# Kernel tuning notes

Hardware: AMD Instinct MI355X
Metric: run time of the kernel (lower is better)

## Reference

```python
import jax, jax.numpy as jnp
import numpy as np

N_NODES = 10000
N_EDGES = 640000
NODE_DIM = 128
EDGE_DIM = 32
OUT_DIM = 128


def setup_inputs() -> dict:
    key = jax.random.key(0)
    k_h, k_e, k_ef, k_w1, k_w2 = jax.random.split(key, 5)
    h = jax.random.normal(k_h, (N_NODES, NODE_DIM), dtype=jnp.float32)
    edge_index = jax.random.randint(k_e, (2, N_EDGES), 0, N_NODES, dtype=jnp.int64)
    edge_features = jax.random.normal(k_ef, (N_EDGES, EDGE_DIM), dtype=jnp.float32)
    in_dim = 2 * NODE_DIM + EDGE_DIM
    # Kaiming-ish init scale for realism
    W1 = jax.random.normal(k_w1, (in_dim, OUT_DIM), dtype=jnp.float32) / np.sqrt(in_dim)
    b1 = jnp.zeros((OUT_DIM,), dtype=jnp.float32)
    W2 = jax.random.normal(k_w2, (OUT_DIM, OUT_DIM), dtype=jnp.float32) / np.sqrt(OUT_DIM)
    b2 = jnp.zeros((OUT_DIM,), dtype=jnp.float32)
    return {"h": h, "edge_index": edge_index, "edge_features": edge_features,
            "n": N_NODES, "W1": W1, "b1": b1, "W2": W2, "b2": b2}


def reference(h, edge_index, edge_features, n, W1, b1, W2, b2):
    rows, cols = edge_index[0], edge_index[1]
    # gather source/target node features + edge features -> [E, 2*node_dim+edge_dim]
    msg_input = jnp.concatenate([h[rows], h[cols], edge_features], axis=-1)
    hidden = jax.nn.relu(msg_input @ W1 + b1)   # [E, out_dim]
    messages = hidden @ W2 + b2                 # [E, out_dim]
    # scatter-add messages onto destination rows -> [n, out_dim]
    out = jax.ops.segment_sum(messages, rows, num_segments=n)
    return out
```

## Files before the change

### kernel.cpp

```cpp
#include <hip/hip_runtime.h>
#include <hip/hip_bf16.h>


typedef __attribute__((ext_vector_type(8))) short bf16x8;
typedef __attribute__((ext_vector_type(4))) float f32x4;

#define ND 128
#define ED 32
#define CH 64

__device__ __forceinline__ short f2bf(float x) {
  unsigned int u = __float_as_uint(x);
  unsigned int r = (u + 0x7FFFu + ((u >> 16) & 1u)) >> 16;
  return (short)r;
}

__device__ __forceinline__ float bf2f(short s) {
  return __uint_as_float(((unsigned int)(unsigned short)s) << 16);
}

__device__ __forceinline__ f32x4 bf8lo(bf16x8 v) {
  f32x4 r;
  #pragma unroll
  for (int j = 0; j < 4; ++j) r[j] = bf2f(v[j]);
  return r;
}
__device__ __forceinline__ f32x4 bf8hi(bf16x8 v) {
  f32x4 r;
  #pragma unroll
  for (int j = 0; j < 4; ++j) r[j] = bf2f(v[4 + j]);
  return r;
}

__device__ __forceinline__ int load_idx(const void* ei, long long i, int is64) {
  return is64 ? (int)((const long long*)ei)[i] : ((const int*)ei)[i];
}

__device__ __forceinline__ int swz(int c) {
  int ct = c >> 4, cc = c & 15;
  return (ct >> 2) * 64 + (cc >> 2) * 16 + (ct & 3) * 4 + (cc & 3);
}

__global__ __launch_bounds__(256) void prep_kernel(
    const float* __restrict__ W1, const float* __restrict__ W2,
    const unsigned int* __restrict__ ei, short* __restrict__ w12t,
    short* __restrict__ w1eA, short* __restrict__ w2t, int* __restrict__ flag) {
  if (blockIdx.x == 0 && threadIdx.x == 0) {
    int is64 = 1;
    for (int i = 0; i < 16; ++i)
      if (ei[2 * i + 1] != 0u) is64 = 0;
    flag[0] = is64;
  }
  int t = blockIdx.x * blockDim.x + threadIdx.x;
  if (t < 256 * 128) {
    int np = t >> 7, k = t & 127;
    float v = (np < 128) ? W1[k * 128 + np] : W1[(128 + k) * 128 + (np - 128)];
    w12t[t] = f2bf(v);
  }
  if (t < 128 * 128) {
    int n = t >> 7, k = t & 127;
    w2t[t] = f2bf(W2[k * 128 + n]);
  }
  if (t < 8 * 64 * 8) {
    int ct = t >> 9, lane = (t >> 3) & 63, j = t & 7;
    int li = lane & 15, lg = lane >> 4;
    w1eA[t] = f2bf(W1[(256 + lg * 8 + j) * 128 + ct * 16 + li]);
  }
}

__global__ void hist_kernel(const void* __restrict__ ei, const int* __restrict__ flag,
                            int* __restrict__ counts, int* __restrict__ rank, int E) {
  int e = blockIdx.x * blockDim.x + threadIdx.x;
  if (e >= E) return;
  int r = load_idx(ei, e, flag[0]);
  rank[e] = atomicAdd(&counts[r], 1);
}

__global__ __launch_bounds__(1024) void scan_kernel(const int* __restrict__ counts,
                                                    int* __restrict__ row_ptr, int n) {
  __shared__ int wtot[16];
  int tid = threadIdx.x;
  int lane = tid & 63, w = tid >> 6;
  int base_i = tid * 16;
  int c[16];
  int tot = 0;
  #pragma unroll
  for (int j = 0; j < 16; ++j) {
    int i = base_i + j;
    c[j] = (i < n) ? counts[i] : 0;
    tot += c[j];
  }
  int x = tot;
  #pragma unroll
  for (int d = 1; d < 64; d <<= 1) {
    int t = __shfl_up(x, d);
    if (lane >= d) x += t;
  }
  if (lane == 63) wtot[w] = x;
  __syncthreads();
  if (w == 0) {
    int y = (lane < 16) ? wtot[lane] : 0;
    #pragma unroll
    for (int d = 1; d < 16; d <<= 1) {
      int t = __shfl_up(y, d);
      if (lane >= d) y += t;
    }
    if (lane < 16) wtot[lane] = y;
  }
  __syncthreads();
  int waveoff = (w == 0) ? 0 : wtot[w - 1];
  int run = waveoff + x - tot;
  if (tid == 0) row_ptr[0] = 0;
  #pragma unroll
  for (int j = 0; j < 16; ++j) {
    int i = base_i + j;
    if (i < n) {
      run += c[j];
      row_ptr[i + 1] = run;
    }
  }
}

__global__ __launch_bounds__(256, 4) void scatter_sg_kernel(
    const void* __restrict__ ei, const int* __restrict__ flag,
    const int* __restrict__ row_ptr, const int* __restrict__ rank,
    const float* __restrict__ h, const short* __restrict__ w12t,
    const float* __restrict__ b1, int2* __restrict__ ec, int2* __restrict__ cb,
    float* __restrict__ s2, short* __restrict__ g2, int N, int E, int nchunks) {
  int b = blockIdx.x;
  int SGB = (N + 63) >> 6;
  int SCB = (E + 255) >> 8;
  if (b < SGB) {
    int lane = threadIdx.x & 63, w = threadIdx.x >> 6;
    int li = lane & 15, lg = lane >> 4;
    int base = b * 64 + w * 16;
    int rowm = base + li;
    if (rowm >= N) rowm = N - 1;
    float breg[8];
    #pragma unroll
    for (int nt = 0; nt < 8; ++nt) breg[nt] = b1[nt * 16 + li];
    f32x4 acc[16];
    #pragma unroll
    for (int nt = 0; nt < 16; ++nt) acc[nt] = (f32x4){0.f, 0.f, 0.f, 0.f};
    #pragma unroll
    for (int kc = 0; kc < 4; ++kc) {
      f32x4 f0 = *(const f32x4*)(h + (size_t)rowm * ND + kc * 32 + lg * 8);
      f32x4 f1 = *(const f32x4*)(h + (size_t)rowm * ND + kc * 32 + lg * 8 + 4);
      bf16x8 a;
      #pragma unroll
      for (int j = 0; j < 4; ++j) { a[j] = f2bf(f0[j]); a[4 + j] = f2bf(f1[j]); }
      #pragma unroll
      for (int nt = 0; nt < 16; ++nt) {
        bf16x8 bb = *(const bf16x8*)(w12t + (nt * 16 + li) * 128 + kc * 32 + lg * 8);
        acc[nt] = __builtin_amdgcn_mfma_f32_16x16x32_bf16(a, bb, acc[nt], 0, 0, 0);
      }
    }
    #pragma unroll
    for (int nt = 0; nt < 16; ++nt)
      #pragma unroll
      for (int r = 0; r < 4; ++r) {
        int row = base + lg * 4 + r;
        if (row < N) {
          if (nt < 8) {
            s2[(size_t)row * 128 + swz(nt * 16 + li)] = acc[nt][r] + breg[nt];
          } else {
            g2[(size_t)row * 128 + swz((nt - 8) * 16 + li)] = f2bf(acc[nt][r]);
          }
        }
      }
  } else if (b < SGB + SCB) {
    int e = (b - SGB) * 256 + threadIdx.x;
    if (e < E) {
      int f = flag[0];
      int r = load_idx(ei, e, f);
      int c = load_idx(ei, (long long)E + e, f);
      ec[row_ptr[r] + rank[e]] = make_int2(e, c);
    }
  } else {
    int k = (b - SGB - SCB) * 256 + threadIdx.x;
    if (k < nchunks) {
      int t0 = k * CH, t1 = t0 + CH;
      int lo = 0, hi = N;
      while (lo < hi) { int mid = (lo + hi) >> 1; if (row_ptr[mid] < t0) lo = mid + 1; else hi = mid; }
      int na = lo;
      hi = N;
      while (lo < hi) { int mid = (lo + hi) >> 1; if (row_ptr[mid] < t1) lo = mid + 1; else hi = mid; }
      cb[k] = make_int2(na, lo);
    }
  }
}

__global__ __launch_bounds__(128) void layer1_kernel(
    const float* __restrict__ s2, const short* __restrict__ g2,
    const float* __restrict__ ef, const int2* __restrict__ ec,
    const short* __restrict__ w1eA, const int* __restrict__ row_ptr,
    const int2* __restrict__ cb, float* __restrict__ hsum) {
  int2 bounds = cb[blockIdx.x];
  int na = bounds.x, nb = bounds.y;
  if (na >= nb) return;
  int lane = threadIdx.x & 63;
  int w = threadIdx.x >> 6;
  int li = lane & 15, lg = lane >> 4;

  bf16x8 wa[4];
  #pragma unroll
  for (int nt = 0; nt < 4; ++nt)
    wa[nt] = *(const bf16x8*)(w1eA + ((w * 4 + nt) * 64 + lane) * 8);

  for (int n = na; n < nb; ++n) {
    int rp = row_ptr[n], rpe = row_ptr[n + 1];
    int deg = rpe - rp;
    f32x4 sreg[4];
    #pragma unroll
    for (int nt = 0; nt < 4; ++nt)
      sreg[nt] = *(const f32x4*)(s2 + (size_t)n * 128 + w * 64 + lg * 16 + nt * 4);
    f32x4 psum[4];
    #pragma unroll
    for (int nt = 0; nt < 4; ++nt) psum[nt] = (f32x4){0.f, 0.f, 0.f, 0.f};

    int ntiles = (deg + 15) >> 4;
    int last = rpe - 1;
    for (int tb = 0; tb < ntiles; tb += 4) {
      int nact = ntiles - tb;
      if (nact > 4) nact = 4;
      int2 ev[4];
      #pragma unroll
      for (int m = 0; m < 4; ++m) {
        int p = rp + (tb + m) * 16 + li;
        ev[m] = ec[p > last ? last : p];
      }
      f32x4 ea[4], eb[4];
      #pragma unroll
      for (int m = 0; m < 4; ++m) {
        const float* ep = ef + (size_t)ev[m].x * ED + lg * 8;
        ea[m] = *(const f32x4*)ep;
        eb[m] = *(const f32x4*)(ep + 4);
      }
      #pragma unroll
      for (int m = 0; m < 4; ++m) {
        if (m < nact) {
          const short* gp = g2 + (size_t)ev[m].y * 128 + w * 64 + lg * 16;
          bf16x8 g0 = *(const bf16x8*)gp;
          bf16x8 g1 = *(const bf16x8*)(gp + 8);
          bf16x8 bfrag;
          #pragma unroll
          for (int j = 0; j < 4; ++j) { bfrag[j] = f2bf(ea[m][j]); bfrag[4 + j] = f2bf(eb[m][j]); }
          f32x4 a0 = __builtin_amdgcn_mfma_f32_16x16x32_bf16(wa[0], bfrag, (f32x4){0.f,0.f,0.f,0.f}, 0, 0, 0);
          f32x4 a1 = __builtin_amdgcn_mfma_f32_16x16x32_bf16(wa[1], bfrag, (f32x4){0.f,0.f,0.f,0.f}, 0, 0, 0);
          f32x4 a2 = __builtin_amdgcn_mfma_f32_16x16x32_bf16(wa[2], bfrag, (f32x4){0.f,0.f,0.f,0.f}, 0, 0, 0);
          f32x4 a3 = __builtin_amdgcn_mfma_f32_16x16x32_bf16(wa[3], bfrag, (f32x4){0.f,0.f,0.f,0.f}, 0, 0, 0);
          if ((tb + m) * 16 + li < deg) {
            f32x4 v0 = a0 + sreg[0] + bf8lo(g0);
            f32x4 v1 = a1 + sreg[1] + bf8hi(g0);
            f32x4 v2 = a2 + sreg[2] + bf8lo(g1);
            f32x4 v3 = a3 + sreg[3] + bf8hi(g1);
            #pragma unroll
            for (int r = 0; r < 4; ++r) {
              psum[0][r] += (v0[r] > 0.f ? v0[r] : 0.f);
              psum[1][r] += (v1[r] > 0.f ? v1[r] : 0.f);
              psum[2][r] += (v2[r] > 0.f ? v2[r] : 0.f);
              psum[3][r] += (v3[r] > 0.f ? v3[r] : 0.f);
            }
          }
        }
      }
    }

    #pragma unroll
    for (int nt = 0; nt < 4; ++nt)
      #pragma unroll
      for (int r = 0; r < 4; ++r) {
        float v = psum[nt][r];
        v += __shfl_xor(v, 1);
        v += __shfl_xor(v, 2);
        v += __shfl_xor(v, 4);
        v += __shfl_xor(v, 8);
        psum[nt][r] = v;
      }
    if (li == 0) {
      #pragma unroll
      for (int nt = 0; nt < 4; ++nt)
        *(f32x4*)(hsum + (size_t)n * 128 + w * 64 + nt * 16 + lg * 4) = psum[nt];
    }
  }
}

__global__ __launch_bounds__(256) void out_kernel(const float* __restrict__ hsum,
                                                  const short* __restrict__ w2t,
                                                  const float* __restrict__ b2,
                                                  const int* __restrict__ row_ptr,
                                                  float* __restrict__ out, int N) {
  int lane = threadIdx.x & 63, w = threadIdx.x >> 6;
  int li = lane & 15, lg = lane >> 4;
  int base = blockIdx.x * 64 + w * 16;
  int rowm = base + li;
  if (rowm >= N) rowm = N - 1;
  float breg[8];
  #pragma unroll
  for (int nt = 0; nt < 8; ++nt) breg[nt] = b2[nt * 16 + li];
  f32x4 acc[8];
  #pragma unroll
  for (int nt = 0; nt < 8; ++nt) acc[nt] = (f32x4){0.f, 0.f, 0.f, 0.f};
  #pragma unroll
  for (int kc = 0; kc < 4; ++kc) {
    f32x4 f0 = *(const f32x4*)(hsum + (size_t)rowm * 128 + kc * 32 + lg * 8);
    f32x4 f1 = *(const f32x4*)(hsum + (size_t)rowm * 128 + kc * 32 + lg * 8 + 4);
    bf16x8 a;
    #pragma unroll
    for (int j = 0; j < 4; ++j) { a[j] = f2bf(f0[j]); a[4 + j] = f2bf(f1[j]); }
    #pragma unroll
    for (int nt = 0; nt < 8; ++nt) {
      bf16x8 bb = *(const bf16x8*)(w2t + (nt * 16 + li) * 128 + kc * 32 + lg * 8);
      acc[nt] = __builtin_amdgcn_mfma_f32_16x16x32_bf16(a, bb, acc[nt], 0, 0, 0);
    }
  }
  #pragma unroll
  for (int r = 0; r < 4; ++r) {
    int row = base + lg * 4 + r;
    if (row < N) {
      float dg = (float)(row_ptr[row + 1] - row_ptr[row]);
      #pragma unroll
      for (int nt = 0; nt < 8; ++nt)
        out[(size_t)row * 128 + nt * 16 + li] = acc[nt][r] + dg * breg[nt];
    }
  }
}

extern "C" void kernel_launch(void* const* d_in, const int* in_sizes, int n_in,
                              void* d_out, int out_size, void* d_ws, size_t ws_size,
                              hipStream_t stream) {
  const float* h  = (const float*)d_in[0];
  const void*  ei = d_in[1];
  const float* ef = (const float*)d_in[2];
  const float* W1 = (const float*)d_in[4];
  const float* b1 = (const float*)d_in[5];
  const float* W2 = (const float*)d_in[6];
  const float* b2 = (const float*)d_in[7];
  float* out = (float*)d_out;
  int N = in_sizes[0] / ND;
  int E = in_sizes[2] / ED;
  int nchunks = (E + CH - 1) / CH;

  char* ws = (char*)d_ws;
  size_t off = 0;
  auto alloc = [&](size_t bytes) {
    size_t o = off;
    off = (off + bytes + 255) & ~(size_t)255;
    return o;
  };
  int*   flag    = (int*)(ws + alloc(4));
  int*   counts  = (int*)(ws + alloc((size_t)N * 4));
  int*   row_ptr = (int*)(ws + alloc((size_t)(N + 1) * 4));
  int*   rank    = (int*)(ws + alloc((size_t)E * 4));
  short* w12t    = (short*)(ws + alloc(256 * 128 * 2));
  short* w1eA    = (short*)(ws + alloc(8 * 64 * 8 * 2));
  short* w2t     = (short*)(ws + alloc(128 * 128 * 2));
  float* s2      = (float*)(ws + alloc((size_t)N * 128 * 4));
  short* g2      = (short*)(ws + alloc((size_t)N * 128 * 2));
  float* hsumb   = (float*)(ws + alloc((size_t)N * 128 * 4));
  int2*  ec      = (int2*)(ws + alloc((size_t)E * 8));
  int2*  cbb     = (int2*)(ws + alloc((size_t)nchunks * 8));

  int SGB = (N + 63) >> 6;
  int SCB = (E + 255) >> 8;
  int CBB = (nchunks + 255) >> 8;

  hipMemsetAsync(counts, 0, (size_t)N * 4, stream);
  prep_kernel<<<128, 256, 0, stream>>>(W1, W2, (const unsigned int*)ei, w12t, w1eA, w2t, flag);
  hist_kernel<<<(E + 255) / 256, 256, 0, stream>>>(ei, flag, counts, rank, E);
  scan_kernel<<<1, 1024, 0, stream>>>(counts, row_ptr, N);
  scatter_sg_kernel<<<SGB + SCB + CBB, 256, 0, stream>>>(
      ei, flag, row_ptr, rank, h, w12t, b1, ec, cbb, s2, g2, N, E, nchunks);
  layer1_kernel<<<nchunks, 128, 0, stream>>>(s2, g2, ef, ec, w1eA, row_ptr, cbb, hsumb);
  out_kernel<<<(N + 63) / 64, 256, 0, stream>>>(hsumb, w2t, b2, row_ptr, out, N);
}
```

Measured before the change: 150.7 us.

## Pre-sort edge features to bf16 in CSR order and software-pipeline layer1 gathers

The scatter pass now writes the edge features converted to bf16 in destination-sorted order, plus 16-bit column indices, so layer1 reads contiguous bf16 rows instead of randomly gathering fp32 features through an (e,c) pair. Layer1 is rewritten as a one-tile-at-a-time loop that prefetches the next two tiles' indices, features and g2 rows, with launch bounds raised for occupancy. The hist kernel packs row and column into one 32-bit word for reuse, and the counts memset is folded into prep_kernel. The packing assumes node ids fit in 16 bits, and the extra sorted-copy write adds traffic to the scatter stage.

```diff
diff --git a/kernel.cpp b/kernel.cpp
--- a/kernel.cpp
+++ b/kernel.cpp
@@ -44,7 +44,8 @@
 __global__ __launch_bounds__(256) void prep_kernel(
     const float* __restrict__ W1, const float* __restrict__ W2,
     const unsigned int* __restrict__ ei, short* __restrict__ w12t,
-    short* __restrict__ w1eA, short* __restrict__ w2t, int* __restrict__ flag) {
+    short* __restrict__ w1eA, short* __restrict__ w2t, int* __restrict__ flag,
+    int* __restrict__ counts, int N) {
   if (blockIdx.x == 0 && threadIdx.x == 0) {
     int is64 = 1;
     for (int i = 0; i < 16; ++i)
@@ -52,6 +53,7 @@
     flag[0] = is64;
   }
   int t = blockIdx.x * blockDim.x + threadIdx.x;
+  for (int i = t; i < N; i += 32768) counts[i] = 0;
   if (t < 256 * 128) {
     int np = t >> 7, k = t & 127;
     float v = (np < 128) ? W1[k * 128 + np] : W1[(128 + k) * 128 + (np - 128)];
@@ -69,11 +71,15 @@
 }
 
 __global__ void hist_kernel(const void* __restrict__ ei, const int* __restrict__ flag,
-                            int* __restrict__ counts, int* __restrict__ rank, int E) {
+                            int* __restrict__ counts, int* __restrict__ rank,
+                            unsigned int* __restrict__ rc, int E) {
   int e = blockIdx.x * blockDim.x + threadIdx.x;
   if (e >= E) return;
-  int r = load_idx(ei, e, flag[0]);
+  int f = flag[0];
+  int r = load_idx(ei, e, f);
+  int c = load_idx(ei, (long long)E + e, f);
   rank[e] = atomicAdd(&counts[r], 1);
+  rc[e] = ((unsigned int)r << 16) | (unsigned int)c;
 }
 
 __global__ __launch_bounds__(1024) void scan_kernel(const int* __restrict__ counts,
@@ -122,14 +128,15 @@
 }
 
 __global__ __launch_bounds__(256, 4) void scatter_sg_kernel(
-    const void* __restrict__ ei, const int* __restrict__ flag,
-    const int* __restrict__ row_ptr, const int* __restrict__ rank,
+    const float* __restrict__ ef, const int* __restrict__ row_ptr,
+    const int* __restrict__ rank, const unsigned int* __restrict__ rc,
     const float* __restrict__ h, const short* __restrict__ w12t,
-    const float* __restrict__ b1, int2* __restrict__ ec, int2* __restrict__ cb,
+    const float* __restrict__ b1, short* __restrict__ efb,
+    unsigned short* __restrict__ ccol, int2* __restrict__ cb,
     float* __restrict__ s2, short* __restrict__ g2, int N, int E, int nchunks) {
   int b = blockIdx.x;
   int SGB = (N + 63) >> 6;
-  int SCB = (E + 255) >> 8;
+  int SCB = (4 * E + 255) >> 8;
   if (b < SGB) {
     int lane = threadIdx.x & 63, w = threadIdx.x >> 6;
     int li = lane & 15, lg = lane >> 4;
@@ -169,12 +176,19 @@
         }
       }
   } else if (b < SGB + SCB) {
-    int e = (b - SGB) * 256 + threadIdx.x;
+    int gt = (b - SGB) * 256 + threadIdx.x;
+    int e = gt >> 2, part = gt & 3;
     if (e < E) {
-      int f = flag[0];
-      int r = load_idx(ei, e, f);
-      int c = load_idx(ei, (long long)E + e, f);
-      ec[row_ptr[r] + rank[e]] = make_int2(e, c);
+      unsigned int p = rc[e];
+      int r = (int)(p >> 16), c = (int)(p & 0xffffu);
+      int pos = row_ptr[r] + rank[e];
+      f32x4 a0 = *(const f32x4*)(ef + (size_t)e * ED + part * 8);
+      f32x4 a1 = *(const f32x4*)(ef + (size_t)e * ED + part * 8 + 4);
+      bf16x8 ob;
+      #pragma unroll
+      for (int j = 0; j < 4; ++j) { ob[j] = f2bf(a0[j]); ob[4 + j] = f2bf(a1[j]); }
+      *(bf16x8*)(efb + (size_t)pos * ED + part * 8) = ob;
+      if (part == 0) ccol[pos] = (unsigned short)c;
     }
   } else {
     int k = (b - SGB - SCB) * 256 + threadIdx.x;
@@ -190,9 +204,9 @@
   }
 }
 
-__global__ __launch_bounds__(128) void layer1_kernel(
+__global__ __launch_bounds__(128, 4) void layer1_kernel(
     const float* __restrict__ s2, const short* __restrict__ g2,
-    const float* __restrict__ ef, const int2* __restrict__ ec,
+    const short* __restrict__ efb, const unsigned short* __restrict__ ccol,
     const short* __restrict__ w1eA, const int* __restrict__ row_ptr,
     const int2* __restrict__ cb, float* __restrict__ hsum) {
   int2 bounds = cb[blockIdx.x];
@@ -220,50 +234,45 @@
 
     int ntiles = (deg + 15) >> 4;
     int last = rpe - 1;
-    for (int tb = 0; tb < ntiles; tb += 4) {
-      int nact = ntiles - tb;
-      if (nact > 4) nact = 4;
-      int2 ev[4];
-      #pragma unroll
-      for (int m = 0; m < 4; ++m) {
-        int p = rp + (tb + m) * 16 + li;
-        ev[m] = ec[p > last ? last : p];
-      }
-      f32x4 ea[4], eb[4];
-      #pragma unroll
-      for (int m = 0; m < 4; ++m) {
-        const float* ep = ef + (size_t)ev[m].x * ED + lg * 8;
-        ea[m] = *(const f32x4*)ep;
-        eb[m] = *(const f32x4*)(ep + 4);
-      }
-      #pragma unroll
-      for (int m = 0; m < 4; ++m) {
-        if (m < nact) {
-          const short* gp = g2 + (size_t)ev[m].y * 128 + w * 64 + lg * 16;
-          bf16x8 g0 = *(const bf16x8*)gp;
-          bf16x8 g1 = *(const bf16x8*)(gp + 8);
-          bf16x8 bfrag;
-          #pragma unroll
-          for (int j = 0; j < 4; ++j) { bfrag[j] = f2bf(ea[m][j]); bfrag[4 + j] = f2bf(eb[m][j]); }
-          f32x4 a0 = __builtin_amdgcn_mfma_f32_16x16x32_bf16(wa[0], bfrag, (f32x4){0.f,0.f,0.f,0.f}, 0, 0, 0);
-          f32x4 a1 = __builtin_amdgcn_mfma_f32_16x16x32_bf16(wa[1], bfrag, (f32x4){0.f,0.f,0.f,0.f}, 0, 0, 0);
-          f32x4 a2 = __builtin_amdgcn_mfma_f32_16x16x32_bf16(wa[2], bfrag, (f32x4){0.f,0.f,0.f,0.f}, 0, 0, 0);
-          f32x4 a3 = __builtin_amdgcn_mfma_f32_16x16x32_bf16(wa[3], bfrag, (f32x4){0.f,0.f,0.f,0.f}, 0, 0, 0);
-          if ((tb + m) * 16 + li < deg) {
-            f32x4 v0 = a0 + sreg[0] + bf8lo(g0);
-            f32x4 v1 = a1 + sreg[1] + bf8hi(g0);
-            f32x4 v2 = a2 + sreg[2] + bf8lo(g1);
-            f32x4 v3 = a3 + sreg[3] + bf8hi(g1);
-            #pragma unroll
-            for (int r = 0; r < 4; ++r) {
-              psum[0][r] += (v0[r] > 0.f ? v0[r] : 0.f);
-              psum[1][r] += (v1[r] > 0.f ? v1[r] : 0.f);
-              psum[2][r] += (v2[r] > 0.f ? v2[r] : 0.f);
-              psum[3][r] += (v3[r] > 0.f ? v3[r] : 0.f);
-            }
-          }
+    auto ldpos = [&](int t) {
+      int p = rp + t * 16 + li;
+      return p > last ? last : p;
+    };
+
+    int pA = ldpos(0), pB = ldpos(1);
+    int cA = ccol[pA], cB = ccol[pB];
+    bf16x8 eA = *(const bf16x8*)(efb + (size_t)pA * ED + lg * 8);
+    bf16x8 eB = *(const bf16x8*)(efb + (size_t)pB * ED + lg * 8);
+    const short* gpA = g2 + (size_t)cA * 128 + w * 64 + lg * 16;
+    bf16x8 gA0 = *(const bf16x8*)gpA;
+    bf16x8 gA1 = *(const bf16x8*)(gpA + 8);
+
+    for (int t = 0; t < ntiles; ++t) {
+      const short* gpB = g2 + (size_t)cB * 128 + w * 64 + lg * 16;
+      bf16x8 gB0 = *(const bf16x8*)gpB;
+      bf16x8 gB1 = *(const bf16x8*)(gpB + 8);
+      int pC = ldpos(t + 2);
+      int cC = ccol[pC];
+      bf16x8 eC = *(const bf16x8*)(efb + (size_t)pC * ED + lg * 8);
+      f32x4 a0 = __builtin_amdgcn_mfma_f32_16x16x32_bf16(wa[0], eA, (f32x4){0.f,0.f,0.f,0.f}, 0, 0, 0);
+      f32x4 a1 = __builtin_amdgcn_mfma_f32_16x16x32_bf16(wa[1], eA, (f32x4){0.f,0.f,0.f,0.f}, 0, 0, 0);
+      f32x4 a2 = __builtin_amdgcn_mfma_f32_16x16x32_bf16(wa[2], eA, (f32x4){0.f,0.f,0.f,0.f}, 0, 0, 0);
+      f32x4 a3 = __builtin_amdgcn_mfma_f32_16x16x32_bf16(wa[3], eA, (f32x4){0.f,0.f,0.f,0.f}, 0, 0, 0);
+      if ((t * 16 + li) < deg) {
+        f32x4 v0 = a0 + sreg[0] + bf8lo(gA0);
+        f32x4 v1 = a1 + sreg[1] + bf8hi(gA0);
+        f32x4 v2 = a2 + sreg[2] + bf8lo(gA1);
+        f32x4 v3 = a3 + sreg[3] + bf8hi(gA1);
+        #pragma unroll
+        for (int r = 0; r < 4; ++r) {
+          psum[0][r] += (v0[r] > 0.f ? v0[r] : 0.f);
+          psum[1][r] += (v1[r] > 0.f ? v1[r] : 0.f);
+          psum[2][r] += (v2[r] > 0.f ? v2[r] : 0.f);
+          psum[3][r] += (v3[r] > 0.f ? v3[r] : 0.f);
         }
       }
+      cB = cC; eA = eB; eB = eC;
+      gA0 = gB0; gA1 = gB1;
     }
 
     #pragma unroll
@@ -348,29 +357,31 @@
     off = (off + bytes + 255) & ~(size_t)255;
     return o;
   };
-  int*   flag    = (int*)(ws + alloc(4));
-  int*   counts  = (int*)(ws + alloc((size_t)N * 4));
-  int*   row_ptr = (int*)(ws + alloc((size_t)(N + 1) * 4));
-  int*   rank    = (int*)(ws + alloc((size_t)E * 4));
-  short* w12t    = (short*)(ws + alloc(256 * 128 * 2));
-  short* w1eA    = (short*)(ws + alloc(8 * 64 * 8 * 2));
-  short* w2t     = (short*)(ws + alloc(128 * 128 * 2));
-  float* s2      = (float*)(ws + alloc((size_t)N * 128 * 4));
-  short* g2      = (short*)(ws + alloc((size_t)N * 128 * 2));
-  float* hsumb   = (float*)(ws + alloc((size_t)N * 128 * 4));
-  int2*  ec      = (int2*)(ws + alloc((size_t)E * 8));
-  int2*  cbb     = (int2*)(ws + alloc((size_t)nchunks * 8));
+  int*            flag    = (int*)(ws + alloc(4));
+  int*            counts  = (int*)(ws + alloc((size_t)N * 4));
+  int*            row_ptr = (int*)(ws + alloc((size_t)(N + 1) * 4));
+  int*            rank    = (int*)(ws + alloc((size_t)E * 4));
+  unsigned int*   rc      = (unsigned int*)(ws + alloc((size_t)E * 4));
+  short*          w12t    = (short*)(ws + alloc(256 * 128 * 2));
+  short*          w1eA    = (short*)(ws + alloc(8 * 64 * 8 * 2));
+  short*          w2t     = (short*)(ws + alloc(128 * 128 * 2));
+  float*          s2      = (float*)(ws + alloc((size_t)N * 128 * 4));
+  short*          g2      = (short*)(ws + alloc((size_t)N * 128 * 2));
+  float*          hsumb   = (float*)(ws + alloc((size_t)N * 128 * 4));
+  short*          efb     = (short*)(ws + alloc((size_t)E * ED * 2));
+  unsigned short* ccol    = (unsigned short*)(ws + alloc((size_t)E * 2));
+  int2*           cbb     = (int2*)(ws + alloc((size_t)nchunks * 8));
 
   int SGB = (N + 63) >> 6;
-  int SCB = (E + 255) >> 8;
+  int SCB = (4 * E + 255) >> 8;
   int CBB = (nchunks + 255) >> 8;
 
-  hipMemsetAsync(counts, 0, (size_t)N * 4, stream);
-  prep_kernel<<<128, 256, 0, stream>>>(W1, W2, (const unsigned int*)ei, w12t, w1eA, w2t, flag);
-  hist_kernel<<<(E + 255) / 256, 256, 0, stream>>>(ei, flag, counts, rank, E);
+  prep_kernel<<<128, 256, 0, stream>>>(W1, W2, (const unsigned int*)ei, w12t, w1eA, w2t,
+                                       flag, counts, N);
+  hist_kernel<<<(E + 255) / 256, 256, 0, stream>>>(ei, flag, counts, rank, rc, E);
   scan_kernel<<<1, 1024, 0, stream>>>(counts, row_ptr, N);
   scatter_sg_kernel<<<SGB + SCB + CBB, 256, 0, stream>>>(
-      ei, flag, row_ptr, rank, h, w12t, b1, ec, cbb, s2, g2, N, E, nchunks);
-  layer1_kernel<<<nchunks, 128, 0, stream>>>(s2, g2, ef, ec, w1eA, row_ptr, cbb, hsumb);
+      ef, row_ptr, rank, rc, h, w12t, b1, efb, ccol, cbb, s2, g2, N, E, nchunks);
+  layer1_kernel<<<nchunks, 128, 0, stream>>>(s2, g2, efb, ccol, w1eA, row_ptr, cbb, hsumb);
   out_kernel<<<(N + 63) / 64, 256, 0, stream>>>(hsumb, w2t, b2, row_ptr, out, N);
 }
```

New measurement: 139.1 us. -7.7%, faster.
